# Optimization experiments

Hardware: AMD Instinct MI355X
Metric: run time of the kernel (lower is better)

Reference implementation:

```python
import jax, jax.numpy as jnp
import numpy as np
import math

B, T, D, H, FFN_DIM, SE_HID = 16, 1024, 512, 8, 2048, 256
EPS = 1e-5  # torch LayerNorm default


def layer_norm(x, g, b):
    mu = jnp.mean(x, axis=-1, keepdims=True)
    var = jnp.mean((x - mu) ** 2, axis=-1, keepdims=True)
    return (x - mu) * jax.lax.rsqrt(var + EPS) * g + b


def setup_inputs() -> dict:
    key = jax.random.key(0)
    ks = jax.random.split(key, 8)
    s = 0.02
    return {
        "x": jax.random.normal(ks[0], (B, T, D), dtype=jnp.float32),
        "wq": jax.random.normal(ks[1], (D, D), dtype=jnp.float32) * s,
        "wk": jax.random.normal(ks[2], (D, D), dtype=jnp.float32) * s,
        "wv": jax.random.normal(ks[3], (D, D), dtype=jnp.float32) * s,
        "ln1_g": jnp.ones((D,), jnp.float32),
        "ln1_b": jnp.zeros((D,), jnp.float32),
        "se_w1": jax.random.normal(ks[4], (T, SE_HID), dtype=jnp.float32) * s,
        "se_w2": jax.random.normal(ks[5], (SE_HID, T), dtype=jnp.float32) * s,
        "ffn_g": jnp.ones((D,), jnp.float32),
        "ffn_b": jnp.zeros((D,), jnp.float32),
        "w1": jax.random.normal(ks[6], (D, FFN_DIM), dtype=jnp.float32) * s,
        "b1": jnp.zeros((FFN_DIM,), jnp.float32),
        "w2": jax.random.normal(ks[7], (FFN_DIM, D), dtype=jnp.float32) * s,
        "b2": jnp.zeros((D,), jnp.float32),
    }


def _forward(x, wq, wk, wv, ln1_g, ln1_b, se_w1, se_w2, ffn_g, ffn_b, w1, b1, w2, b2):
    # --- SE gate over the sequence axis: squeeze over feature dim D ---
    y = jnp.mean(x, axis=-1)                       # (B, T)
    gate = jax.nn.sigmoid(jax.nn.relu(y @ se_w1) @ se_w2)  # (B, T)
    x = x + x * gate[..., None]

    d = D // H
    n = layer_norm(x, ln1_g, ln1_b)
    q = (n @ wq).reshape(B, T, H, d)
    k = (n @ wk).reshape(B, T, H, d)
    v = (n @ wv).reshape(B, T, H, d)
    attn = jnp.einsum('bnhd,bmhd->bnmh', q, k) / math.sqrt(d)
    w = jax.nn.softmax(attn, axis=2)               # softmax over key dim m
    x = x + jnp.einsum('bnmh,bmhd->bnhd', w, v).reshape(B, T, D)

    # --- FFN (pre-norm, exact GELU as nn.GELU default) ---
    n2 = layer_norm(x, ffn_g, ffn_b)
    h = jax.nn.gelu(n2 @ w1 + b1, approximate=False)
    return x + (h @ w2 + b2)


def reference(x, wq, wk, wv, ln1_g, ln1_b, se_w1, se_w2, ffn_g, ffn_b, w1, b1, w2, b2):
    return _forward(x, wq, wk, wv, ln1_g, ln1_b, se_w1, se_w2, ffn_g, ffn_b, w1, b1, w2, b2)
```

## Files before the change

### kernel.cpp

```cpp
#include <hip/hip_runtime.h>

typedef unsigned int uint32;

using bf16x8 = __attribute__((ext_vector_type(8))) short;
using f32x4  = __attribute__((ext_vector_type(4))) float;

#define B_  16
#define T_  1024
#define D_  512
#define H_  8
#define HD_ 64
#define FFN_ 2048
#define SEH_ 256
#define EPS_ 1e-5f
#define PS_ 80

#define AS1 __attribute__((address_space(1)))
#define AS3 __attribute__((address_space(3)))

__device__ __forceinline__ ushort f2bf(float f) {
  uint32 x = __float_as_uint(f);
  return (ushort)((x + 0x7fffu + ((x >> 16) & 1u)) >> 16);
}
__device__ __forceinline__ float bf2f(ushort u) {
  return __uint_as_float(((uint32)u) << 16);
}
__device__ __forceinline__ float gelu_fast(float v) {
  float u = v * (0.7978845608f + 0.0356774081f * v * v);
  float e = __expf(2.0f * u);
  float t = 1.0f - 2.0f * __builtin_amdgcn_rcpf(e + 1.0f);
  return 0.5f * v * (1.0f + t);
}

__global__ __launch_bounds__(256) void cast_transpose_all_k(
    const float* __restrict__ wq, const float* __restrict__ wk,
    const float* __restrict__ wv, const float* __restrict__ w1,
    const float* __restrict__ w2, ushort* __restrict__ wqkvT,
    ushort* __restrict__ w1T, ushort* __restrict__ w2T) {
  __shared__ float tile[32][33];
  int bid = blockIdx.x;
  const float* W; ushort* WT; int K, N, bk, bn;
  if (bid < 768) {
    int w = bid >> 8, r = bid & 255;
    W = (w == 0) ? wq : (w == 1) ? wk : wv;
    WT = wqkvT + (size_t)w * 512 * 512;
    K = 512; N = 512; bk = (r >> 4) * 32; bn = (r & 15) * 32;
  } else if (bid < 1792) {
    int r = bid - 768;
    W = w1; WT = w1T; K = 512; N = 2048; bk = (r >> 6) * 32; bn = (r & 63) * 32;
  } else {
    int r = bid - 1792;
    W = w2; WT = w2T; K = 2048; N = 512; bk = (r >> 4) * 32; bn = (r & 15) * 32;
  }
  int lx = threadIdx.x & 31;
  int ly = threadIdx.x >> 5;
  #pragma unroll
  for (int i = ly; i < 32; i += 8)
    tile[i][lx] = W[(size_t)(bk + i) * N + bn + lx];
  __syncthreads();
  #pragma unroll
  for (int i = ly; i < 32; i += 8)
    WT[(size_t)(bn + i) * K + bk + lx] = f2bf(tile[lx][i]);
}

__global__ __launch_bounds__(256) void se_rowmean_k(const float* __restrict__ x,
                                                    float* __restrict__ y) {
  int row  = blockIdx.x * 4 + (threadIdx.x >> 6);
  int lane = threadIdx.x & 63;
  const float4* p = (const float4*)(x + (size_t)row * D_);
  float4 a = p[lane * 2];
  float4 b = p[lane * 2 + 1];
  float s = a.x + a.y + a.z + a.w + b.x + b.y + b.z + b.w;
  #pragma unroll
  for (int m = 1; m < 64; m <<= 1) s += __shfl_xor(s, m);
  if (lane == 0) y[row] = s * (1.0f / D_);
}

__global__ __launch_bounds__(256) void se_mlp1_k(const float* __restrict__ y,
                                                 const float* __restrict__ w1,
                                                 float* __restrict__ z) {
  __shared__ float yb[T_];
  __shared__ float part[8][32];
  int b = blockIdx.x, jt = blockIdx.y;
  int tid = threadIdx.x;
  #pragma unroll
  for (int i = 0; i < 4; i++) yb[tid + i * 256] = y[(size_t)b * T_ + tid + i * 256];
  __syncthreads();
  int tj = tid & 31, tk = tid >> 5;
  int j = jt * 32 + tj;
  const float* wp = w1 + (size_t)(tk * 128) * SEH_ + j;
  const float* yp = yb + tk * 128;
  float a0 = 0.f, a1 = 0.f, a2 = 0.f, a3 = 0.f;
  #pragma unroll
  for (int t = 0; t < 128; t += 4) {
    a0 += yp[t]     * wp[(t)     * SEH_];
    a1 += yp[t + 1] * wp[(t + 1) * SEH_];
    a2 += yp[t + 2] * wp[(t + 2) * SEH_];
    a3 += yp[t + 3] * wp[(t + 3) * SEH_];
  }
  part[tk][tj] = (a0 + a1) + (a2 + a3);
  __syncthreads();
  if (tid < 32) {
    float s = 0.f;
    #pragma unroll
    for (int k = 0; k < 8; k++) s += part[k][tid];
    z[(size_t)b * SEH_ + jt * 32 + tid] = fmaxf(s, 0.f);
  }
}

__global__ __launch_bounds__(256) void se_mlp2_k(const float* __restrict__ z,
                                                 const float* __restrict__ w2,
                                                 float* __restrict__ gate) {
  __shared__ float zb[SEH_];
  __shared__ float part[2][128];
  int b = blockIdx.x, bt = blockIdx.y;
  int tid = threadIdx.x;
  zb[tid & 255] = z[(size_t)b * SEH_ + (tid & 255)];
  __syncthreads();
  int tt = tid & 127, tk = tid >> 7;
  int t = bt * 128 + tt;
  const float* wp = w2 + (size_t)(tk * 128) * T_ + t;
  const float* zp = zb + tk * 128;
  float a0 = 0.f, a1 = 0.f, a2 = 0.f, a3 = 0.f;
  #pragma unroll
  for (int j = 0; j < 128; j += 4) {
    a0 += zp[j]     * wp[(j)     * T_];
    a1 += zp[j + 1] * wp[(j + 1) * T_];
    a2 += zp[j + 2] * wp[(j + 2) * T_];
    a3 += zp[j + 3] * wp[(j + 3) * T_];
  }
  part[tk][tt] = (a0 + a1) + (a2 + a3);
  __syncthreads();
  if (tid < 128) {
    float s = part[0][tid] + part[1][tid];
    gate[(size_t)b * T_ + bt * 128 + tid] = 1.0f / (1.0f + __expf(-s));
  }
}

__global__ __launch_bounds__(256) void gate_ln1_k(
    const float* __restrict__ x, const float* __restrict__ gate,
    const float* __restrict__ g, const float* __restrict__ beta,
    float* __restrict__ x1, ushort* __restrict__ nbuf) {
  int rid  = blockIdx.x * 4 + (threadIdx.x >> 6);
  int lane = threadIdx.x & 63;
  const float4* xr = (const float4*)(x + (size_t)rid * D_);
  float4 a = xr[lane * 2];
  float4 b = xr[lane * 2 + 1];
  float gv = 1.0f + gate[rid];
  a.x *= gv; a.y *= gv; a.z *= gv; a.w *= gv;
  b.x *= gv; b.y *= gv; b.z *= gv; b.w *= gv;
  float4* x1r = (float4*)(x1 + (size_t)rid * D_);
  x1r[lane * 2]     = a;
  x1r[lane * 2 + 1] = b;
  float s  = a.x + a.y + a.z + a.w + b.x + b.y + b.z + b.w;
  float ss = a.x*a.x + a.y*a.y + a.z*a.z + a.w*a.w + b.x*b.x + b.y*b.y + b.z*b.z + b.w*b.w;
  #pragma unroll
  for (int m = 1; m < 64; m <<= 1) { s += __shfl_xor(s, m); ss += __shfl_xor(ss, m); }
  float mu   = s * (1.0f / D_);
  float var  = ss * (1.0f / D_) - mu * mu;
  float rstd = rsqrtf(var + EPS_);
  const float4* gp = (const float4*)g;
  const float4* bp = (const float4*)beta;
  float4 g0 = gp[lane * 2], g1 = gp[lane * 2 + 1];
  float4 b0 = bp[lane * 2], b1 = bp[lane * 2 + 1];
  union { uint4 v; ushort u[8]; } pk;
  pk.u[0] = f2bf((a.x - mu) * rstd * g0.x + b0.x);
  pk.u[1] = f2bf((a.y - mu) * rstd * g0.y + b0.y);
  pk.u[2] = f2bf((a.z - mu) * rstd * g0.z + b0.z);
  pk.u[3] = f2bf((a.w - mu) * rstd * g0.w + b0.w);
  pk.u[4] = f2bf((b.x - mu) * rstd * g1.x + b1.x);
  pk.u[5] = f2bf((b.y - mu) * rstd * g1.y + b1.y);
  pk.u[6] = f2bf((b.z - mu) * rstd * g1.z + b1.z);
  pk.u[7] = f2bf((b.w - mu) * rstd * g1.w + b1.w);
  *(uint4*)(nbuf + (size_t)rid * D_ + lane * 8) = pk.v;
}

__global__ __launch_bounds__(256) void ln2_k(
    const float* __restrict__ x2, const float* __restrict__ g,
    const float* __restrict__ beta, ushort* __restrict__ nbuf) {
  int rid  = blockIdx.x * 4 + (threadIdx.x >> 6);
  int lane = threadIdx.x & 63;
  const float4* xr = (const float4*)(x2 + (size_t)rid * D_);
  float4 a = xr[lane * 2];
  float4 b = xr[lane * 2 + 1];
  float s  = a.x + a.y + a.z + a.w + b.x + b.y + b.z + b.w;
  float ss = a.x*a.x + a.y*a.y + a.z*a.z + a.w*a.w + b.x*b.x + b.y*b.y + b.z*b.z + b.w*b.w;
  #pragma unroll
  for (int m = 1; m < 64; m <<= 1) { s += __shfl_xor(s, m); ss += __shfl_xor(ss, m); }
  float mu   = s * (1.0f / D_);
  float var  = ss * (1.0f / D_) - mu * mu;
  float rstd = rsqrtf(var + EPS_);
  const float4* gp = (const float4*)g;
  const float4* bp = (const float4*)beta;
  float4 g0 = gp[lane * 2], g1 = gp[lane * 2 + 1];
  float4 b0 = bp[lane * 2], b1 = bp[lane * 2 + 1];
  union { uint4 v; ushort u[8]; } pk;
  pk.u[0] = f2bf((a.x - mu) * rstd * g0.x + b0.x);
  pk.u[1] = f2bf((a.y - mu) * rstd * g0.y + b0.y);
  pk.u[2] = f2bf((a.z - mu) * rstd * g0.z + b0.z);
  pk.u[3] = f2bf((a.w - mu) * rstd * g0.w + b0.w);
  pk.u[4] = f2bf((b.x - mu) * rstd * g1.x + b1.x);
  pk.u[5] = f2bf((b.y - mu) * rstd * g1.y + b1.y);
  pk.u[6] = f2bf((b.z - mu) * rstd * g1.z + b1.z);
  pk.u[7] = f2bf((b.w - mu) * rstd * g1.w + b1.w);
  *(uint4*)(nbuf + (size_t)rid * D_ + lane * 8) = pk.v;
}

#define MFMA16 __builtin_amdgcn_mfma_f32_16x16x32_bf16
template <int BN>
__global__ __launch_bounds__(512, 2) void gemm256_k(
    const ushort* __restrict__ A, const ushort* __restrict__ BT,
    int M, int N, int K,
    const float* __restrict__ bias, const float* __restrict__ resid,
    ushort* __restrict__ outB, ushort* __restrict__ outB2,
    ushort* __restrict__ vTout, float* __restrict__ outF, int epi) {
  constexpr int WNS   = BN / 4;
  constexpr int NT    = BN / 64;
  constexpr int NH    = NT / 2;
  constexpr int BROWS = BN / 8;
  constexpr int BJ    = BN / 64;
  __shared__ ushort smem[2 * 256 * 64 + 2 * BN * 64];
  ushort* As = smem;
  ushort* Bs = smem + 2 * 256 * 64;

  int tid  = threadIdx.x;
  int wave = tid >> 6;
  int lane = tid & 63;
  int quad = lane >> 4;
  int l15  = lane & 15;
  int wm   = wave >> 2;
  int wn   = wave & 3;
  int lr   = lane >> 3;
  int lcs  = (lane & 7) ^ lr;

  int nbk = N / BN;
  int bid = blockIdx.x;
  int xcd = bid & 7;
  int sb  = bid >> 3;
  int n0  = (sb % nbk) * BN;
  int m0  = ((sb / nbk) * 8 + xcd) * 256;

  f32x4 acc[8][NT];
  #pragma unroll
  for (int i = 0; i < 8; i++)
    #pragma unroll
    for (int j = 0; j < NT; j++) acc[i][j] = (f32x4){0.f, 0.f, 0.f, 0.f};

  const ushort* Ag = A  + (size_t)(m0 + wave * 32 + lr) * K + lcs * 8;
  const ushort* Bg = BT + (size_t)(n0 + wave * BROWS + lr) * K + lcs * 8;

  auto STAGE = [&](int t, int buf) {
    int ko = t * 64;
    ushort* da = As + buf * (256 * 64) + wave * (32 * 64);
    #pragma unroll
    for (int j = 0; j < 4; j++)
      __builtin_amdgcn_global_load_lds((const AS1 void*)(Ag + ko + (size_t)(j * 8) * K),
                                       (AS3 void*)(da + j * 512), 16, 0, 0);
    ushort* db = Bs + buf * (BN * 64) + wave * (BROWS * 64);
    #pragma unroll
    for (int j = 0; j < BJ; j++)
      __builtin_amdgcn_global_load_lds((const AS1 void*)(Bg + ko + (size_t)(j * 8) * K),
                                       (AS3 void*)(db + j * 512), 16, 0, 0);
  };

  int ntt = K >> 6;
  STAGE(0, 0);
  STAGE(1, 1);
  if constexpr (BN == 256) asm volatile("s_waitcnt vmcnt(8)" ::: "memory");
  else                     asm volatile("s_waitcnt vmcnt(6)" ::: "memory");
  __builtin_amdgcn_s_barrier();

  const ushort* Arow = As + (wm * 128 + l15) * 64;
  const ushort* Brow = Bs + (wn * WNS + l15) * 64;
  int c0 = ((0 + quad) ^ (l15 & 7)) * 8;
  int c1 = ((4 + quad) ^ (l15 & 7)) * 8;

  for (int t = 0; t < ntt; ++t) {
    const ushort* Ab = Arow + (t & 1) * (256 * 64);
    const ushort* Bb = Brow + (t & 1) * (BN * 64);
    bf16x8 a[4][2], b[NT][2];

    #pragma unroll
    for (int m4 = 0; m4 < 4; m4++) {
      a[m4][0] = *(const bf16x8*)(Ab + m4 * 1024 + c0);
      a[m4][1] = *(const bf16x8*)(Ab + m4 * 1024 + c1);
    }
    #pragma unroll
    for (int h = 0; h < NH; h++) {
      b[h][0] = *(const bf16x8*)(Bb + h * 1024 + c0);
      b[h][1] = *(const bf16x8*)(Bb + h * 1024 + c1);
    }
    __builtin_amdgcn_s_barrier();
    asm volatile("s_waitcnt lgkmcnt(0)" ::: "memory");
    __builtin_amdgcn_sched_barrier(0);
    __builtin_amdgcn_s_setprio(1);
    #pragma unroll
    for (int m4 = 0; m4 < 4; m4++)
      #pragma unroll
      for (int h = 0; h < NH; h++) {
        acc[m4][h] = MFMA16(a[m4][0], b[h][0], acc[m4][h], 0, 0, 0);
        acc[m4][h] = MFMA16(a[m4][1], b[h][1], acc[m4][h], 0, 0, 0);
      }
    __builtin_amdgcn_s_setprio(0);
    __builtin_amdgcn_s_barrier();

    #pragma unroll
    for (int h = 0; h < NH; h++) {
      b[NH + h][0] = *(const bf16x8*)(Bb + (NH + h) * 1024 + c0);
      b[NH + h][1] = *(const bf16x8*)(Bb + (NH + h) * 1024 + c1);
    }
    __builtin_amdgcn_s_barrier();
    asm volatile("s_waitcnt lgkmcnt(0)" ::: "memory");
    __builtin_amdgcn_sched_barrier(0);
    __builtin_amdgcn_s_setprio(1);
    #pragma unroll
    for (int m4 = 0; m4 < 4; m4++)
      #pragma unroll
      for (int h = 0; h < NH; h++) {
        acc[m4][NH + h] = MFMA16(a[m4][0], b[NH + h][0], acc[m4][NH + h], 0, 0, 0);
        acc[m4][NH + h] = MFMA16(a[m4][1], b[NH + h][1], acc[m4][NH + h], 0, 0, 0);
      }
    __builtin_amdgcn_s_setprio(0);
    __builtin_amdgcn_s_barrier();

    #pragma unroll
    for (int m4 = 0; m4 < 4; m4++) {
      a[m4][0] = *(const bf16x8*)(Ab + (4 + m4) * 1024 + c0);
      a[m4][1] = *(const bf16x8*)(Ab + (4 + m4) * 1024 + c1);
    }
    __builtin_amdgcn_s_barrier();
    asm volatile("s_waitcnt lgkmcnt(0)" ::: "memory");
    __builtin_amdgcn_sched_barrier(0);
    __builtin_amdgcn_s_setprio(1);
    #pragma unroll
    for (int m4 = 0; m4 < 4; m4++)
      #pragma unroll
      for (int h = 0; h < NH; h++) {
        acc[4 + m4][h] = MFMA16(a[m4][0], b[h][0], acc[4 + m4][h], 0, 0, 0);
        acc[4 + m4][h] = MFMA16(a[m4][1], b[h][1], acc[4 + m4][h], 0, 0, 0);
      }
    __builtin_amdgcn_s_setprio(0);
    __builtin_amdgcn_s_barrier();

    __builtin_amdgcn_s_setprio(1);
    #pragma unroll
    for (int m4 = 0; m4 < 4; m4++)
      #pragma unroll
      for (int h = 0; h < NH; h++) {
        acc[4 + m4][NH + h] = MFMA16(a[m4][0], b[NH + h][0], acc[4 + m4][NH + h], 0, 0, 0);
        acc[4 + m4][NH + h] = MFMA16(a[m4][1], b[NH + h][1], acc[4 + m4][NH + h], 0, 0, 0);
      }
    __builtin_amdgcn_s_setprio(0);

    if (t + 1 < ntt) {
      if (t + 2 < ntt) {
        STAGE(t + 2, t & 1);
        if constexpr (BN == 256) asm volatile("s_waitcnt vmcnt(8)" ::: "memory");
        else                     asm volatile("s_waitcnt vmcnt(6)" ::: "memory");
      } else {
        asm volatile("s_waitcnt vmcnt(0)" ::: "memory");
      }
      __builtin_amdgcn_s_barrier();
    }
  }

  int colbase = n0 + wn * WNS;
  if (epi == 2) {
    #pragma unroll
    for (int nt = 0; nt < NT; nt++) {
      int n = colbase + nt * 16 + l15;
      float bv = bias[n];
      #pragma unroll
      for (int mt = 0; mt < 8; mt++) {
        int m = m0 + wm * 128 + mt * 16 + quad * 4;
        #pragma unroll
        for (int r = 0; r < 4; r++) {
          size_t idx = (size_t)(m + r) * N + n;
          outF[idx] = acc[mt][nt][r] + bv + resid[idx];
        }
      }
    }
  } else {
    __syncthreads();
    if (epi == 3 && n0 >= 1024) {
      constexpr int TST = 136;
      ushort* tb = smem + wave * (32 * TST);
      #pragma unroll
      for (int nt = 0; nt < NT; nt++) {
        int dloc = nt * 16 + l15;
        #pragma unroll
        for (int mt = 0; mt < 8; mt++) {
          ushort4 pk;
          pk.x = f2bf(acc[mt][nt][0]);
          pk.y = f2bf(acc[mt][nt][1]);
          pk.z = f2bf(acc[mt][nt][2]);
          pk.w = f2bf(acc[mt][nt][3]);
          *(ushort4*)(tb + dloc * TST + mt * 16 + quad * 4) = pk;
        }
      }
      int dbase = (n0 - 1024) + wn * WNS;
      int bb = m0 >> 10;
      int tg = (m0 & 1023) + wm * 128 + l15 * 8;
      #pragma unroll
      for (int j = 0; j < 8; j++) {
        int dloc = j * 4 + quad;
        int d = dbase + dloc;
        int hh = d >> 6, dd = d & 63;
        uint4 vv = *(const uint4*)(tb + dloc * TST + l15 * 8);
        *(uint4*)(vTout + (((size_t)bb * 8 + hh) * 64 + dd) * 1024 + tg) = vv;
      }
    } else {
      constexpr int RS  = WNS + 8;
      constexpr int LPR = WNS / 8;
      constexpr int RPS = 64 / LPR;
      ushort* tb = smem + wave * (32 * RS);
      ushort* gout; int ldN; float scl;
      if (epi == 1) { gout = outB; ldN = N; scl = 1.0f; }
      else { gout = (n0 < 512) ? outB : outB2; ldN = 512; scl = (n0 < 512) ? 0.125f : 1.0f; }
      int ncol = (epi == 1) ? colbase : ((n0 & 511) + wn * WNS);
      float bv[NT];
      #pragma unroll
      for (int nt = 0; nt < NT; nt++)
        bv[nt] = (epi == 1) ? bias[colbase + nt * 16 + l15] : 0.0f;
      int rrow = lane / LPR;
      int seg  = lane % LPR;
      int mrow0 = m0 + wm * 128;
      #pragma unroll
      for (int mtg = 0; mtg < 4; mtg++) {
        #pragma unroll
        for (int mh = 0; mh < 2; mh++) {
          int mt = mtg * 2 + mh;
          #pragma unroll
          for (int nt = 0; nt < NT; nt++) {
            #pragma unroll
            for (int r = 0; r < 4; r++) {
              float v = (epi == 1) ? gelu_fast(acc[mt][nt][r] + bv[nt])
                                   : acc[mt][nt][r] * scl;
              tb[(mh * 16 + quad * 4 + r) * RS + nt * 16 + l15] = f2bf(v);
            }
          }
        }
        #pragma unroll
        for (int it = 0; it < 32 / RPS; it++) {
          int rl = it * RPS + rrow;
          uint4 v = *(const uint4*)(tb + rl * RS + seg * 8);
          *(uint4*)(gout + (size_t)(mrow0 + mtg * 32 + rl) * ldN + ncol + seg * 8) = v;
        }
      }
    }
  }
}

__global__ __launch_bounds__(256) void attn_k(
    const ushort* __restrict__ q, const ushort* __restrict__ k,
    const ushort* __restrict__ vT, const float* __restrict__ x1,
    float* __restrict__ out) {
  __shared__ ushort Ks[64 * PS_];
  __shared__ ushort Vs[64 * PS_];
  __shared__ ushort Ps[128 * PS_];
  int blk = blockIdx.x;
  int qt = blk & 7;
  int h  = (blk >> 3) & 7;
  int b  = blk >> 6;
  int t0 = qt * 128;
  int tid  = threadIdx.x;
  int wave = tid >> 6;
  int lane = tid & 63;
  int quad = lane >> 4;
  int l15  = lane & 15;

  const ushort* qp0 = q + ((size_t)(b * T_ + t0 + wave * 16 + l15)) * D_ + h * HD_;
  const ushort* qp1 = qp0 + (size_t)64 * D_;
  bf16x8 aq0 = *(const bf16x8*)(qp0 + quad * 8);
  bf16x8 aq1 = *(const bf16x8*)(qp0 + 32 + quad * 8);
  bf16x8 aq2 = *(const bf16x8*)(qp1 + quad * 8);
  bf16x8 aq3 = *(const bf16x8*)(qp1 + 32 + quad * 8);

  int srow = tid >> 2;
  int scol = (tid & 3) * 16;

  float l_part[2][4] = {{0.f, 0.f, 0.f, 0.f}, {0.f, 0.f, 0.f, 0.f}};
  f32x4 o0[4], o1[4];
  #pragma unroll
  for (int dt = 0; dt < 4; dt++) {
    o0[dt] = (f32x4){0.f, 0.f, 0.f, 0.f};
    o1[dt] = (f32x4){0.f, 0.f, 0.f, 0.f};
  }

  const ushort* vTb = vT + ((size_t)(b * 8 + h) * 64 + srow) * 1024 + scol;

  for (int kt = 0; kt < 16; kt++) {
    size_t kgbase = ((size_t)(b * T_ + kt * 64 + srow)) * D_ + h * HD_ + scol;
    uint4 ku0 = *(const uint4*)(k + kgbase);
    uint4 ku1 = *(const uint4*)(k + kgbase + 8);
    const ushort* vp = vTb + kt * 64;
    uint4 vv0 = *(const uint4*)(vp);
    uint4 vv1 = *(const uint4*)(vp + 8);

    __syncthreads();

    *(uint4*)(Ks + srow * PS_ + scol)     = ku0;
    *(uint4*)(Ks + srow * PS_ + scol + 8) = ku1;
    *(uint4*)(Vs + srow * PS_ + scol)     = vv0;
    *(uint4*)(Vs + srow * PS_ + scol + 8) = vv1;

    __syncthreads();

    f32x4 s0[4], s1[4];
    #pragma unroll
    for (int nt = 0; nt < 4; nt++) {
      bf16x8 bk0 = *(const bf16x8*)(Ks + (nt * 16 + l15) * PS_ + quad * 8);
      bf16x8 bk1 = *(const bf16x8*)(Ks + (nt * 16 + l15) * PS_ + 32 + quad * 8);
      f32x4 z = (f32x4){0.f, 0.f, 0.f, 0.f};
      s0[nt] = __builtin_amdgcn_mfma_f32_16x16x32_bf16(aq0, bk0, z, 0, 0, 0);
      s0[nt] = __builtin_amdgcn_mfma_f32_16x16x32_bf16(aq1, bk1, s0[nt], 0, 0, 0);
      s1[nt] = __builtin_amdgcn_mfma_f32_16x16x32_bf16(aq2, bk0, z, 0, 0, 0);
      s1[nt] = __builtin_amdgcn_mfma_f32_16x16x32_bf16(aq3, bk1, s1[nt], 0, 0, 0);
    }

    #pragma unroll
    for (int nt = 0; nt < 4; nt++) {
      int pcol = nt * 16 + l15;
      int prow0 = (wave * 16 + quad * 4) * PS_ + pcol;
      #pragma unroll
      for (int r = 0; r < 4; r++) {
        float p0 = __expf(s0[nt][r]);
        float p1 = __expf(s1[nt][r]);
        l_part[0][r] += p0;
        l_part[1][r] += p1;
        Ps[prow0 + r * PS_]            = f2bf(p0);
        Ps[prow0 + (64 + r) * PS_]     = f2bf(p1);
      }
    }

    bf16x8 ap0 = *(const bf16x8*)(Ps + (wave * 16 + l15) * PS_ + quad * 8);
    bf16x8 ap1 = *(const bf16x8*)(Ps + (wave * 16 + l15) * PS_ + 32 + quad * 8);
    bf16x8 ap2 = *(const bf16x8*)(Ps + (64 + wave * 16 + l15) * PS_ + quad * 8);
    bf16x8 ap3 = *(const bf16x8*)(Ps + (64 + wave * 16 + l15) * PS_ + 32 + quad * 8);
    #pragma unroll
    for (int dt = 0; dt < 4; dt++) {
      bf16x8 bv0 = *(const bf16x8*)(Vs + (dt * 16 + l15) * PS_ + quad * 8);
      bf16x8 bv1 = *(const bf16x8*)(Vs + (dt * 16 + l15) * PS_ + 32 + quad * 8);
      o0[dt] = __builtin_amdgcn_mfma_f32_16x16x32_bf16(ap0, bv0, o0[dt], 0, 0, 0);
      o0[dt] = __builtin_amdgcn_mfma_f32_16x16x32_bf16(ap1, bv1, o0[dt], 0, 0, 0);
      o1[dt] = __builtin_amdgcn_mfma_f32_16x16x32_bf16(ap2, bv0, o1[dt], 0, 0, 0);
      o1[dt] = __builtin_amdgcn_mfma_f32_16x16x32_bf16(ap3, bv1, o1[dt], 0, 0, 0);
    }
  }

  #pragma unroll
  for (int s = 0; s < 2; s++) {
    f32x4* oo = s ? o1 : o0;
    #pragma unroll
    for (int r = 0; r < 4; r++) {
      float l = l_part[s][r];
      l += __shfl_xor(l, 1);
      l += __shfl_xor(l, 2);
      l += __shfl_xor(l, 4);
      l += __shfl_xor(l, 8);
      float inv = 1.0f / l;
      int qrow = t0 + s * 64 + wave * 16 + quad * 4 + r;
      size_t base = ((size_t)(b * T_ + qrow)) * D_ + h * HD_;
      #pragma unroll
      for (int dt = 0; dt < 4; dt++) {
        size_t idx = base + dt * 16 + l15;
        out[idx] = x1[idx] + oo[dt][r] * inv;
      }
    }
  }
}

extern "C" void kernel_launch(void* const* d_in, const int* in_sizes, int n_in,
                              void* d_out, int out_size, void* d_ws, size_t ws_size,
                              hipStream_t stream) {
  (void)in_sizes; (void)n_in; (void)out_size; (void)ws_size;
  const float* x     = (const float*)d_in[0];
  const float* wq    = (const float*)d_in[1];
  const float* wk    = (const float*)d_in[2];
  const float* wv    = (const float*)d_in[3];
  const float* ln1_g = (const float*)d_in[4];
  const float* ln1_b = (const float*)d_in[5];
  const float* se_w1 = (const float*)d_in[6];
  const float* se_w2 = (const float*)d_in[7];
  const float* ffn_g = (const float*)d_in[8];
  const float* ffn_b = (const float*)d_in[9];
  const float* w1    = (const float*)d_in[10];
  const float* b1    = (const float*)d_in[11];
  const float* w2    = (const float*)d_in[12];
  const float* b2    = (const float*)d_in[13];
  float* out = (float*)d_out;
  char* ws = (char*)d_ws;

  constexpr size_t X1_OFF   = 0;
  constexpr size_t N_OFF    = 33554432;
  constexpr size_t Q_OFF    = 50331648;
  constexpr size_t K_OFF    = 67108864;
  constexpr size_t V_OFF    = 83886080;
  constexpr size_t H_OFF    = 50331648;
  constexpr size_t WQKV_OFF = 117440512;
  constexpr size_t W1T_OFF  = 119013376;
  constexpr size_t W2T_OFF  = 121110528;
  constexpr size_t Y_OFF    = 123207680;
  constexpr size_t Z_OFF    = 123273216;
  constexpr size_t GATE_OFF = 123289600;

  float*  x1    = (float*)(ws + X1_OFF);
  ushort* nbuf  = (ushort*)(ws + N_OFF);
  ushort* qb    = (ushort*)(ws + Q_OFF);
  ushort* kb    = (ushort*)(ws + K_OFF);
  ushort* vT    = (ushort*)(ws + V_OFF);
  ushort* hb    = (ushort*)(ws + H_OFF);
  ushort* wqkvT = (ushort*)(ws + WQKV_OFF);
  ushort* w1T   = (ushort*)(ws + W1T_OFF);
  ushort* w2T   = (ushort*)(ws + W2T_OFF);
  float*  yv    = (float*)(ws + Y_OFF);
  float*  zv    = (float*)(ws + Z_OFF);
  float*  gate  = (float*)(ws + GATE_OFF);

  const int M = B_ * T_;

  cast_transpose_all_k<<<2816, 256, 0, stream>>>(wq, wk, wv, w1, w2, wqkvT, w1T, w2T);

  se_rowmean_k<<<M / 4, 256, 0, stream>>>(x, yv);
  se_mlp1_k<<<dim3(B_, 8), 256, 0, stream>>>(yv, se_w1, zv);
  se_mlp2_k<<<dim3(B_, 8), 256, 0, stream>>>(zv, se_w2, gate);

  gate_ln1_k<<<M / 4, 256, 0, stream>>>(x, gate, ln1_g, ln1_b, x1, nbuf);

  gemm256_k<128><<<(M / 256) * (1536 / 128), 512, 0, stream>>>(
      nbuf, wqkvT, M, 1536, D_, nullptr, nullptr, qb, kb, vT, nullptr, 3);

  attn_k<<<B_ * H_ * (T_ / 128), 256, 0, stream>>>(qb, kb, vT, x1, out);

  ln2_k<<<M / 4, 256, 0, stream>>>(out, ffn_g, ffn_b, nbuf);

  gemm256_k<256><<<(M / 256) * (FFN_ / 256), 512, 0, stream>>>(
      nbuf, w1T, M, FFN_, D_, b1, nullptr, hb, nullptr, nullptr, nullptr, 1);
  gemm256_k<128><<<(M / 256) * (D_ / 128), 512, 0, stream>>>(
      hb, w2T, M, D_, FFN_, b2, out, nullptr, nullptr, nullptr, out, 2);
}
```

Before: 337.9 us.

## Swizzle attention LDS tiles, prefetch next K/V tile, remap blocks to XCDs, use exp2

The attention kernel replaces padded shared-memory tiles with XOR-swizzled 64-wide tiles for K, V and P. It also register-prefetches the next K/V tile while the current one is being computed, and remaps block indices so that all blocks of a (batch, head) pair land on the same XCD. The Q scale is folded to include log2(e) so that softmax can use the native exp2 instruction. The goals are to cut LDS bank conflicts, hide global load latency and improve L2 locality, at the cost of more register pressure and index arithmetic. MFMA16 is used but its definition does not appear in the shown hunks, so it may be defined elsewhere.

```diff
diff --git a/kernel.cpp b/kernel.cpp
--- a/kernel.cpp
+++ b/kernel.cpp
@@ -13,7 +13,6 @@
 #define FFN_ 2048
 #define SEH_ 256
 #define EPS_ 1e-5f
-#define PS_ 80
 
 #define AS1 __attribute__((address_space(1)))
 #define AS3 __attribute__((address_space(3)))
@@ -416,7 +415,10 @@
       ushort* tb = smem + wave * (32 * RS);
       ushort* gout; int ldN; float scl;
       if (epi == 1) { gout = outB; ldN = N; scl = 1.0f; }
-      else { gout = (n0 < 512) ? outB : outB2; ldN = 512; scl = (n0 < 512) ? 0.125f : 1.0f; }
+      else {
+        gout = (n0 < 512) ? outB : outB2; ldN = 512;
+        scl = (n0 < 512) ? 0.18033688011112042f : 1.0f;
+      }
       int ncol = (epi == 1) ? colbase : ((n0 & 511) + wn * WNS);
       float bv[NT];
       #pragma unroll
@@ -455,13 +457,16 @@
     const ushort* __restrict__ q, const ushort* __restrict__ k,
     const ushort* __restrict__ vT, const float* __restrict__ x1,
     float* __restrict__ out) {
-  __shared__ ushort Ks[64 * PS_];
-  __shared__ ushort Vs[64 * PS_];
-  __shared__ ushort Ps[128 * PS_];
-  int blk = blockIdx.x;
-  int qt = blk & 7;
-  int h  = (blk >> 3) & 7;
-  int b  = blk >> 6;
+  __shared__ ushort Ks[64 * 64];
+  __shared__ ushort Vs[64 * 64];
+  __shared__ ushort Ps[128 * 64];
+  int bid = blockIdx.x;
+  int xcd = bid & 7;
+  int j   = bid >> 3;
+  int qt  = j & 7;
+  int pair = xcd * 16 + (j >> 3);
+  int b = pair >> 3;
+  int h = pair & 7;
   int t0 = qt * 128;
   int tid  = threadIdx.x;
   int wave = tid >> 6;
@@ -477,7 +482,13 @@
   bf16x8 aq3 = *(const bf16x8*)(qp1 + 32 + quad * 8);
 
   int srow = tid >> 2;
-  int scol = (tid & 3) * 16;
+  int c2   = (tid & 3) * 2;
+  int scol = c2 * 8;
+  int sw0  = ((c2)     ^ (srow & 7)) << 3;
+  int sw1  = ((c2 + 1) ^ (srow & 7)) << 3;
+  int swb  = srow * 64;
+  int rsw0 = ((quad)     ^ (l15 & 7)) << 3;
+  int rsw1 = ((quad + 4) ^ (l15 & 7)) << 3;
 
   float l_part[2][4] = {{0.f, 0.f, 0.f, 0.f}, {0.f, 0.f, 0.f, 0.f}};
   f32x4 o0[4], o1[4];
@@ -488,63 +499,75 @@
   }
 
   const ushort* vTb = vT + ((size_t)(b * 8 + h) * 64 + srow) * 1024 + scol;
+  size_t kgb = ((size_t)(b * T_ + srow)) * D_ + h * HD_ + scol;
+
+  uint4 ku0 = *(const uint4*)(k + kgb);
+  uint4 ku1 = *(const uint4*)(k + kgb + 8);
+  uint4 vv0 = *(const uint4*)(vTb);
+  uint4 vv1 = *(const uint4*)(vTb + 8);
 
   for (int kt = 0; kt < 16; kt++) {
-    size_t kgbase = ((size_t)(b * T_ + kt * 64 + srow)) * D_ + h * HD_ + scol;
-    uint4 ku0 = *(const uint4*)(k + kgbase);
-    uint4 ku1 = *(const uint4*)(k + kgbase + 8);
-    const ushort* vp = vTb + kt * 64;
-    uint4 vv0 = *(const uint4*)(vp);
-    uint4 vv1 = *(const uint4*)(vp + 8);
-
     __syncthreads();
 
-    *(uint4*)(Ks + srow * PS_ + scol)     = ku0;
-    *(uint4*)(Ks + srow * PS_ + scol + 8) = ku1;
-    *(uint4*)(Vs + srow * PS_ + scol)     = vv0;
-    *(uint4*)(Vs + srow * PS_ + scol + 8) = vv1;
+    *(uint4*)(Ks + swb + sw0) = ku0;
+    *(uint4*)(Ks + swb + sw1) = ku1;
+    *(uint4*)(Vs + swb + sw0) = vv0;
+    *(uint4*)(Vs + swb + sw1) = vv1;
 
     __syncthreads();
 
+    if (kt + 1 < 16) {
+      size_t kg2 = kgb + (size_t)(kt + 1) * 64 * D_;
+      const ushort* vp2 = vTb + (kt + 1) * 64;
+      ku0 = *(const uint4*)(k + kg2);
+      ku1 = *(const uint4*)(k + kg2 + 8);
+      vv0 = *(const uint4*)(vp2);
+      vv1 = *(const uint4*)(vp2 + 8);
+    }
+
     f32x4 s0[4], s1[4];
     #pragma unroll
     for (int nt = 0; nt < 4; nt++) {
-      bf16x8 bk0 = *(const bf16x8*)(Ks + (nt * 16 + l15) * PS_ + quad * 8);
-      bf16x8 bk1 = *(const bf16x8*)(Ks + (nt * 16 + l15) * PS_ + 32 + quad * 8);
+      const ushort* krow = Ks + (nt * 16 + l15) * 64;
+      bf16x8 bk0 = *(const bf16x8*)(krow + rsw0);
+      bf16x8 bk1 = *(const bf16x8*)(krow + rsw1);
       f32x4 z = (f32x4){0.f, 0.f, 0.f, 0.f};
-      s0[nt] = __builtin_amdgcn_mfma_f32_16x16x32_bf16(aq0, bk0, z, 0, 0, 0);
-      s0[nt] = __builtin_amdgcn_mfma_f32_16x16x32_bf16(aq1, bk1, s0[nt], 0, 0, 0);
-      s1[nt] = __builtin_amdgcn_mfma_f32_16x16x32_bf16(aq2, bk0, z, 0, 0, 0);
-      s1[nt] = __builtin_amdgcn_mfma_f32_16x16x32_bf16(aq3, bk1, s1[nt], 0, 0, 0);
+      s0[nt] = MFMA16(aq0, bk0, z, 0, 0, 0);
+      s0[nt] = MFMA16(aq1, bk1, s0[nt], 0, 0, 0);
+      s1[nt] = MFMA16(aq2, bk0, z, 0, 0, 0);
+      s1[nt] = MFMA16(aq3, bk1, s1[nt], 0, 0, 0);
     }
 
     #pragma unroll
     for (int nt = 0; nt < 4; nt++) {
-      int pcol = nt * 16 + l15;
-      int prow0 = (wave * 16 + quad * 4) * PS_ + pcol;
+      int cps = nt * 2 + (l15 >> 3);
       #pragma unroll
       for (int r = 0; r < 4; r++) {
-        float p0 = __expf(s0[nt][r]);
-        float p1 = __expf(s1[nt][r]);
+        int rowl = quad * 4 + r;
+        int off = (wave * 16 + rowl) * 64 + ((cps ^ (rowl & 7)) << 3) + (l15 & 7);
+        float p0 = __builtin_amdgcn_exp2f(s0[nt][r]);
+        float p1 = __builtin_amdgcn_exp2f(s1[nt][r]);
         l_part[0][r] += p0;
         l_part[1][r] += p1;
-        Ps[prow0 + r * PS_]            = f2bf(p0);
-        Ps[prow0 + (64 + r) * PS_]     = f2bf(p1);
-      }
-    }
-
-    bf16x8 ap0 = *(const bf16x8*)(Ps + (wave * 16 + l15) * PS_ + quad * 8);
-    bf16x8 ap1 = *(const bf16x8*)(Ps + (wave * 16 + l15) * PS_ + 32 + quad * 8);
-    bf16x8 ap2 = *(const bf16x8*)(Ps + (64 + wave * 16 + l15) * PS_ + quad * 8);
-    bf16x8 ap3 = *(const bf16x8*)(Ps + (64 + wave * 16 + l15) * PS_ + 32 + quad * 8);
+        Ps[off]            = f2bf(p0);
+        Ps[off + 64 * 64]  = f2bf(p1);
+      }
+    }
+
+    const ushort* prow = Ps + (wave * 16 + l15) * 64;
+    bf16x8 ap0 = *(const bf16x8*)(prow + rsw0);
+    bf16x8 ap1 = *(const bf16x8*)(prow + rsw1);
+    bf16x8 ap2 = *(const bf16x8*)(prow + 4096 + rsw0);
+    bf16x8 ap3 = *(const bf16x8*)(prow + 4096 + rsw1);
     #pragma unroll
     for (int dt = 0; dt < 4; dt++) {
-      bf16x8 bv0 = *(const bf16x8*)(Vs + (dt * 16 + l15) * PS_ + quad * 8);
-      bf16x8 bv1 = *(const bf16x8*)(Vs + (dt * 16 + l15) * PS_ + 32 + quad * 8);
-      o0[dt] = __builtin_amdgcn_mfma_f32_16x16x32_bf16(ap0, bv0, o0[dt], 0, 0, 0);
-      o0[dt] = __builtin_amdgcn_mfma_f32_16x16x32_bf16(ap1, bv1, o0[dt], 0, 0, 0);
-      o1[dt] = __builtin_amdgcn_mfma_f32_16x16x32_bf16(ap2, bv0, o1[dt], 0, 0, 0);
-      o1[dt] = __builtin_amdgcn_mfma_f32_16x16x32_bf16(ap3, bv1, o1[dt], 0, 0, 0);
+      const ushort* vrow = Vs + (dt * 16 + l15) * 64;
+      bf16x8 bv0 = *(const bf16x8*)(vrow + rsw0);
+      bf16x8 bv1 = *(const bf16x8*)(vrow + rsw1);
+      o0[dt] = MFMA16(ap0, bv0, o0[dt], 0, 0, 0);
+      o0[dt] = MFMA16(ap1, bv1, o0[dt], 0, 0, 0);
+      o1[dt] = MFMA16(ap2, bv0, o1[dt], 0, 0, 0);
+      o1[dt] = MFMA16(ap3, bv1, o1[dt], 0, 0, 0);
     }
   }
 
```

Result: slower. 344.7 us (+2.0%).
